# Kernel optimization log

Hardware: AMD Instinct MI355X
Metric: run time of the kernel (lower is better)

## Reference

```python
import jax, jax.numpy as jnp
import numpy as np

B, N, H = 8, 2000, 64  # batch, num_nodes(=input_dim), hidden(num_gru_units)


def _laplacian_self_loop(a):
    # batched: norm = D^{-1/2} (A + I) D^{-1/2}
    m = a + jnp.eye(a.shape[-1], dtype=a.dtype)
    d_inv_sqrt = jnp.sum(m, axis=-1) ** -0.5  # (B, N)
    return d_inv_sqrt[..., :, None] * m * d_inv_sqrt[..., None, :]


def _graph_conv(inputs, hidden_flat, adj, windd, W2, b2, W3, b3, W, b, out_dim):
    b_, _, n = inputs.shape
    # dynamic wind-based adjacency
    wind_now = inputs[:, 2, :] * 360.0  # (B, N)
    direction = jnp.abs(windd[None, :, :] - wind_now[:, :, None])  # (B, N, N)
    direction = jnp.where(direction > 360.0, 180.0, direction)
    d1 = jnp.maximum(jnp.cos(direction * (jnp.pi / 180.0)), 0.0)
    a = d1 @ W2.T + b2 + (adj @ W3.T + b3)[None]  # (B, N, N)
    a1 = _laplacian_self_loop(jnp.maximum(a, 0.0))
    # graph conv: concat [x, h] then A @ [.] then Linear
    x = jnp.concatenate([inputs[:, 0, :, None], hidden_flat.reshape(b_, n, H)], axis=2)  # (B,N,H+1)
    y = jnp.einsum('bij,bjh->bih', a1, x) @ W.T + b  # (B, N, out_dim)
    return y.reshape(b_, n * out_dim)


def reference(inputs, hidden_state, adj, windd, W2, b2, W3, b3, W1a, b1a, W1b, b1b, Wca1, Wca2, Wsa):
    b_, _, n = inputs.shape
    conc = _graph_conv(inputs, hidden_state, adj, windd, W2, b2, W3, b3, W1a, b1a, 2 * H)
    conc = conc.reshape(b_, 2 * H, n)  # faithful reshape (input_dim == N)
    # --- channel attention (CBAM) ---
    avg = jnp.mean(conc, axis=2, keepdims=True)  # (B, 2H, 1)
    mx = jnp.max(conc, axis=2, keepdims=True)
    def fc(v):
        return jnp.einsum('oc,bcx->box', Wca2, jax.nn.relu(jnp.einsum('oc,bcx->box', Wca1, v)))
    ca = jax.nn.sigmoid(fc(avg) + fc(mx))  # (B, 2H, 1)
    conc = ca * conc
    # --- spatial attention ---
    s = jnp.stack([jnp.mean(conc, axis=1), jnp.max(conc, axis=1)], axis=1)  # (B, 2, N)
    sa = jax.lax.conv_general_dilated(s, Wsa, window_strides=(1,), padding=((3, 3),),
                                      dimension_numbers=('NCH', 'OIH', 'NCH'))  # (B,1,N)
    conc = jax.nn.sigmoid(sa) * conc
    # --- GRU gates ---
    conc = jax.nn.sigmoid(conc.reshape(b_, 2 * H * n))
    r, u = jnp.split(conc, 2, axis=1)  # each (B, N*H)
    c = jnp.tanh(_graph_conv(inputs, r * hidden_state, adj, windd, W2, b2, W3, b3, W1b, b1b, H))
    new_hidden_state = u * hidden_state + (1.0 - u) * c
    return new_hidden_state


def setup_inputs() -> dict:
    key = jax.random.key(0)
    ks = jax.random.split(key, 12)
    inputs = jax.random.uniform(ks[0], (B, 3, N), dtype=jnp.float32)
    hidden_state = jax.random.normal(ks[1], (B, N * H), dtype=jnp.float32) * 0.1
    adj = jax.random.uniform(ks[2], (N, N), dtype=jnp.float32)
    windd = jax.random.uniform(ks[3], (N, N), dtype=jnp.float32) * 360.0
    sN = 1.0 / np.sqrt(N)
    W2 = jax.random.normal(ks[4], (N, N), dtype=jnp.float32) * sN
    b2 = jnp.zeros((N,), jnp.float32)
    W3 = jax.random.normal(ks[5], (N, N), dtype=jnp.float32) * sN
    b3 = jnp.zeros((N,), jnp.float32)
    sI = 1.0 / np.sqrt(H + 1)
    W1a = jax.random.normal(ks[6], (2 * H, H + 1), dtype=jnp.float32) * sI
    b1a = jnp.ones((2 * H,), jnp.float32)  # bias=1.0 in graph_conv1
    W1b = jax.random.normal(ks[7], (H, H + 1), dtype=jnp.float32) * sI
    b1b = jnp.zeros((H,), jnp.float32)
    Wca1 = jax.random.normal(ks[8], (2 * H // 16, 2 * H), dtype=jnp.float32) * (1.0 / np.sqrt(2 * H))
    Wca2 = jax.random.normal(ks[9], (2 * H, 2 * H // 16), dtype=jnp.float32) * (1.0 / np.sqrt(2 * H // 16))
    Wsa = jax.random.normal(ks[10], (1, 2, 7), dtype=jnp.float32) * (1.0 / np.sqrt(14))
    return {'inputs': inputs, 'hidden_state': hidden_state, 'adj': adj, 'windd': windd,
            'W2': W2, 'b2': b2, 'W3': W3, 'b3': b3, 'W1a': W1a, 'b1a': b1a,
            'W1b': W1b, 'b1b': b1b, 'Wca1': Wca1, 'Wca2': Wca2, 'Wsa': Wsa}
```

## Files before the change

kernel.cpp:

```cpp
#include <hip/hip_runtime.h>

#define NN 2000
#define BB 8
#define P  2048
#define NKT 64

typedef __attribute__((ext_vector_type(8))) short bf16x8;
typedef __attribute__((ext_vector_type(4))) float f32x4;

__device__ __forceinline__ float sigf(float x) { return 1.0f / (1.0f + expf(-x)); }

__device__ __forceinline__ short f2bf(float x) {
    union { float f; unsigned u; } v; v.f = x;
    unsigned r = v.u + 0x7fffu + ((v.u >> 16) & 1u);
    return (short)(r >> 16);
}
__device__ __forceinline__ float bf2f(short h) {
    union { unsigned u; float f; } v; v.u = ((unsigned)(unsigned short)h) << 16; return v.f;
}

__device__ __forceinline__ void gl2lds16(const short* g, short* l) {
    __builtin_amdgcn_global_load_lds(
        (const __attribute__((address_space(1))) void*)g,
        (__attribute__((address_space(3))) void*)l, 16, 0, 0);
}

__global__ __launch_bounds__(256) void k_cvtW(
    const float* __restrict__ s0, const float* __restrict__ s1, const float* __restrict__ s2,
    short* __restrict__ d0, short* __restrict__ d1, short* __restrict__ d2)
{
    const int i = blockIdx.x, sel = blockIdx.y, t = threadIdx.x;
    const float* s = (sel == 0) ? s0 : (sel == 1) ? s1 : s2;
    short* d = ((sel == 0) ? d0 : (sel == 1) ? d1 : d2) + ((size_t)i) * P + t * 8;
    bf16x8 v;
#pragma unroll
    for (int e = 0; e < 8; ++e) v[e] = 0;
    if (i < NN && t < 250) {
        const float* p = s + (size_t)i * NN + t * 8;
        float4 x0 = *(const float4*)p;
        float4 x1 = *(const float4*)(p + 4);
        float a[8] = {x0.x,x0.y,x0.z,x0.w,x1.x,x1.y,x1.z,x1.w};
#pragma unroll
        for (int e = 0; e < 8; ++e) v[e] = f2bf(a[e]);
    }
    *(bf16x8*)d = v;
}

__global__ __launch_bounds__(256) void k_cvtD1(
    const float* __restrict__ windd, const float* __restrict__ inputs, short* __restrict__ d1bf)
{
    const int i = blockIdx.x, t = threadIdx.x;
    const bool live = (i < NN) && (t < 250);
    float a[8];
    if (live) {
        const float* p = windd + (size_t)i * NN + t * 8;
        float4 x0 = *(const float4*)p;
        float4 x1 = *(const float4*)(p + 4);
        a[0]=x0.x; a[1]=x0.y; a[2]=x0.z; a[3]=x0.w;
        a[4]=x1.x; a[5]=x1.y; a[6]=x1.z; a[7]=x1.w;
    }
#pragma unroll
    for (int b = 0; b < BB; ++b) {
        bf16x8 v;
#pragma unroll
        for (int e = 0; e < 8; ++e) v[e] = 0;
        if (live) {
            const float wn = inputs[(size_t)b * 3 * NN + 2 * NN + i] * 360.0f;
#pragma unroll
            for (int e = 0; e < 8; ++e) {
                float dd = fabsf(a[e] - wn);
                dd = (dd > 360.0f) ? 180.0f : dd;
                float c = __cosf(dd * 0.01745329251994329577f);
                v[e] = f2bf(fmaxf(c, 0.0f));
            }
        }
        *(bf16x8*)(d1bf + ((size_t)b * P + i) * P + t * 8) = v;
    }
}

__global__ __launch_bounds__(512, 2) void k_g4s(
    const short* __restrict__ d1bf, const short* __restrict__ W2bf,
    const float* __restrict__ b2, const short* __restrict__ adjw,
    short* __restrict__ m_bf)
{
    __shared__ char smem[131072];
    const int t = threadIdx.x;
    const int w = t >> 6, lane = t & 63;
    const int wm = w >> 2, wn = w & 3;
    const int lr = lane & 15, lq = lane >> 4;
    const int tile = blockIdx.x;
    const int b = blockIdx.y;
    const int i0 = (tile & 7) * 256;
    const int j0 = (tile >> 3) * 256;
    const short* A  = d1bf + (size_t)b * P * P;
    const short* Bm = W2bf;

    const int cA0 = w * 64 + lane, cA1 = cA0 + 512;
    const int rA0 = cA0 >> 2, rA1 = cA1 >> 2;
    const short* srcA0 = A + (size_t)(i0 + rA0) * P + (((cA0 & 3) ^ ((rA0 >> 2) & 3)) * 8);
    const short* srcA1 = A + (size_t)(i0 + rA1) * P + (((cA1 & 3) ^ ((rA1 >> 2) & 3)) * 8);
    const short* srcB0 = Bm + (size_t)(j0 + rA0) * P + (((cA0 & 3) ^ ((rA0 >> 2) & 3)) * 8);
    const short* srcB1 = Bm + (size_t)(j0 + rA1) * P + (((cA1 & 3) ^ ((rA1 >> 2) & 3)) * 8);

#define STAGE_A(slot, ktI) do {                                                   \
        gl2lds16(srcA0 + (ktI) * 32, (short*)(smem + (slot) * 16384 + w * 1024)); \
        gl2lds16(srcA1 + (ktI) * 32, (short*)(smem + (slot) * 16384 + 8192 + w * 1024)); } while (0)
#define STAGE_B(slot, ktI) do {                                                   \
        gl2lds16(srcB0 + (ktI) * 32, (short*)(smem + 65536 + (slot) * 16384 + w * 1024)); \
        gl2lds16(srcB1 + (ktI) * 32, (short*)(smem + 65536 + (slot) * 16384 + 8192 + w * 1024)); } while (0)

    const int fch = (lq ^ (lr >> 2)) << 4;
    const int arowB = (wm * 128 + lr) * 64 + fch;
    const int browB = (wn * 64 + lr) * 64 + fch;

    f32x4 acc[8][4];
#pragma unroll
    for (int m = 0; m < 8; ++m)
#pragma unroll
        for (int n = 0; n < 4; ++n) acc[m][n] = (f32x4){0.f, 0.f, 0.f, 0.f};
    bf16x8 aF[4], bF[4];

    STAGE_A(0, 0); STAGE_B(0, 0);
    STAGE_A(1, 1); STAGE_B(1, 1);
    STAGE_A(2, 2); STAGE_B(2, 2);
    asm volatile("s_waitcnt vmcnt(0)" ::: "memory");
    __builtin_amdgcn_s_barrier();
    asm volatile("" ::: "memory");

#define MFMA_(a_, b_, m, n) acc[m][n] = __builtin_amdgcn_mfma_f32_16x16x32_bf16(a_, b_, acc[m][n], 0, 0, 0)
#define PHASE_MID()                                      \
    __builtin_amdgcn_s_barrier();                        \
    asm volatile("s_waitcnt lgkmcnt(0)" ::: "memory");   \
    __builtin_amdgcn_sched_barrier(0);                   \
    __builtin_amdgcn_s_setprio(1)
#define PHASE_TAIL()                                     \
    __builtin_amdgcn_s_setprio(0);                       \
    __builtin_amdgcn_sched_barrier(0);                   \
    asm volatile("s_waitcnt vmcnt(8)" ::: "memory");     \
    __builtin_amdgcn_s_barrier();                        \
    asm volatile("" ::: "memory")

    for (int kt = 0; kt < NKT; ++kt) {
        char* curA = smem + (kt & 3) * 16384;
        char* curB = smem + 65536 + (kt & 3) * 16384;
        const int stgSlot = (kt + 3) & 3;
        const int stgKt = (kt + 3 < NKT) ? (kt + 3) : (NKT - 1);

#pragma unroll
        for (int m = 0; m < 4; ++m) aF[m] = *(const bf16x8*)(curA + arowB + m * 1024);
#pragma unroll
        for (int n = 0; n < 4; ++n) bF[n] = *(const bf16x8*)(curB + browB + n * 1024);
        STAGE_A(stgSlot, stgKt);
        PHASE_MID();
#pragma unroll
        for (int m = 0; m < 4; ++m)
#pragma unroll
            for (int n = 0; n < 4; ++n) MFMA_(aF[m], bF[n], m, n);
        PHASE_TAIL();

#pragma unroll
        for (int m = 0; m < 4; ++m) aF[m] = *(const bf16x8*)(curA + arowB + (m + 4) * 1024);
        STAGE_B(stgSlot, stgKt);
        PHASE_MID();
#pragma unroll
        for (int m = 0; m < 4; ++m)
#pragma unroll
            for (int n = 0; n < 4; ++n) MFMA_(aF[m], bF[n], m + 4, n);
        PHASE_TAIL();
    }
    asm volatile("s_waitcnt vmcnt(0)" ::: "memory");

    const int rbase = i0 + wm * 128 + lq * 4;
    const int cbase = j0 + wn * 64 + lr;
#pragma unroll
    for (int m = 0; m < 8; ++m) {
#pragma unroll
        for (int n = 0; n < 4; ++n) {
            const int col = cbase + n * 16;
#pragma unroll
            for (int q = 0; q < 4; ++q) {
                const int row = rbase + m * 16 + q;
                short o = 0;
                if (row < NN && col < NN) {
                    float x = acc[m][n][q] + b2[col] + bf2f(adjw[(size_t)row * NN + col]);
                    x = fmaxf(x, 0.0f);
                    if (row == col) x += 1.0f;
                    o = f2bf(x);
                }
                m_bf[((size_t)b * P + row) * P + col] = o;
            }
        }
    }
#undef MFMA_
#undef PHASE_MID
#undef PHASE_TAIL
#undef STAGE_A
#undef STAGE_B
}

template<int EPI, int OUTD>
__global__ __launch_bounds__(256) void k_mfma(
    const short* __restrict__ Abase, const short* __restrict__ Bbase,
    const float* __restrict__ bias, const short* __restrict__ adjw,
    void* __restrict__ Cout, float* __restrict__ part, size_t aBatch)
{
    __shared__ short shA[4096];
    __shared__ short shB[4096];
    const int t = threadIdx.x;
    const int w = t >> 6, lane = t & 63;
    const int wr = w >> 1, wc = w & 1;

    int i0, j0, b, kt = 0;
    if (EPI == 2) {
        i0 = blockIdx.x * 128; j0 = 0; kt = blockIdx.y; b = blockIdx.z;
    } else {
        i0 = blockIdx.x * 128; j0 = blockIdx.y * 128; b = 0;
    }
    const int kb = (EPI == 2) ? kt * (P / 4) : 0;
    const int ke = (EPI == 2) ? kt * (P / 4) + (P / 4) : P;

    const short* A  = Abase + (size_t)b * aBatch;
    const short* Bm = Bbase + ((EPI == 2) ? (size_t)b * 128 * P : (size_t)0);

    f32x4 acc[4][4];
#pragma unroll
    for (int m = 0; m < 4; ++m)
#pragma unroll
        for (int n = 0; n < 4; ++n) acc[m][n] = (f32x4){0.f, 0.f, 0.f, 0.f};

    const int lidx0 = w * 128 + lane;
    const int lidx1 = lidx0 + 64;
    const short* aS0 = A  + (size_t)(i0 + (lidx0 >> 2)) * P + (lidx0 & 3) * 8;
    const short* aS1 = A  + (size_t)(i0 + (lidx1 >> 2)) * P + (lidx1 & 3) * 8;
    const short* bS0 = Bm + (size_t)(j0 + (lidx0 >> 2)) * P + (lidx0 & 3) * 8;
    const short* bS1 = Bm + (size_t)(j0 + (lidx1 >> 2)) * P + (lidx1 & 3) * 8;
    short* ldA0 = shA + (w * 128) * 8;
    short* ldA1 = shA + (w * 128 + 64) * 8;
    short* ldB0 = shB + (w * 128) * 8;
    short* ldB1 = shB + (w * 128 + 64) * 8;

    const int lr = lane & 15, lq = lane >> 4;
    const int aoff = (wr * 64 + lr) * 32 + lq * 8;
    const int boff = (wc * 64 + lr) * 32 + lq * 8;

    for (int k0 = kb; k0 < ke; k0 += 32) {
        gl2lds16(aS0 + k0, ldA0);
        gl2lds16(aS1 + k0, ldA1);
        gl2lds16(bS0 + k0, ldB0);
        gl2lds16(bS1 + k0, ldB1);
        __syncthreads();
        bf16x8 aF[4], bF[4];
#pragma unroll
        for (int m = 0; m < 4; ++m) aF[m] = *(const bf16x8*)(shA + aoff + m * 512);
#pragma unroll
        for (int n = 0; n < 4; ++n) bF[n] = *(const bf16x8*)(shB + boff + n * 512);
#pragma unroll
        for (int m = 0; m < 4; ++m)
#pragma unroll
            for (int n = 0; n < 4; ++n)
                acc[m][n] = __builtin_amdgcn_mfma_f32_16x16x32_bf16(aF[m], bF[n], acc[m][n], 0, 0, 0);
        __syncthreads();
    }

    const int rbase = i0 + wr * 64 + lq * 4;
    const int cbase = j0 + wc * 64 + lr;
#pragma unroll
    for (int m = 0; m < 4; ++m) {
#pragma unroll
        for (int n = 0; n < 4; ++n) {
            const int col = cbase + n * 16;
#pragma unroll
            for (int q = 0; q < 4; ++q) {
                const int row = rbase + m * 16 + q;
                float v = acc[m][n][q];
                if (EPI == 0) {
                    if (row < NN && col < NN)
                        ((short*)Cout)[(size_t)row * NN + col] = f2bf(v + bias[col]);
                } else {
                    if (row < NN && col < OUTD)
                        part[((size_t)(kt * BB + b) * NN + row) * OUTD + col] = v;
                }
            }
        }
    }
}

template<int OUTD>
__global__ __launch_bounds__(256) void k_comb(
    const float* __restrict__ part, const float* __restrict__ dinv,
    const float* __restrict__ bias, float* __restrict__ out)
{
    const size_t idx = (size_t)blockIdx.x * 256 + threadIdx.x;
    const size_t S = (size_t)BB * NN * OUTD;
    if (idx >= S) return;
    const int o = (int)(idx % OUTD);
    const size_t r = idx / OUTD;
    const int i = (int)(r % NN);
    const int b = (int)(r / NN);
    float s = ((part[idx] + part[idx + S]) + (part[idx + 2 * S] + part[idx + 3 * S]));
    out[idx] = s * dinv[b * NN + i] + bias[o];
}

__global__ __launch_bounds__(256) void k_rowsum_bf(const short* __restrict__ m_bf, float* __restrict__ dinv)
{
    const int i = blockIdx.x, b = blockIdx.y;
    const short* p = m_bf + ((size_t)b * P + i) * P + threadIdx.x * 8;
    bf16x8 v = *(const bf16x8*)p;
    float s = 0.0f;
#pragma unroll
    for (int e = 0; e < 8; ++e) s += bf2f(v[e]);
#pragma unroll
    for (int off = 32; off > 0; off >>= 1) s += __shfl_down(s, off);
    __shared__ float red[4];
    if ((threadIdx.x & 63) == 0) red[threadIdx.x >> 6] = s;
    __syncthreads();
    if (threadIdx.x == 0) dinv[b * NN + i] = rsqrtf(red[0] + red[1] + red[2] + red[3]);
}

template<int OUT>
__global__ __launch_bounds__(128) void k_xwT(
    const float* __restrict__ inputs, const float* __restrict__ hsrc,
    const float* __restrict__ W, const float* __restrict__ dinv, short* __restrict__ zT)
{
    const int b = blockIdx.y;
    const int j0 = blockIdx.x * 16;
    const int t = threadIdx.x;
    __shared__ float wl[128 * 65];
    __shared__ float xs[16 * 66];
    __shared__ float dj[16];
    for (int idx = t; idx < OUT * 65; idx += 128) wl[idx] = W[idx];
    for (int idx = t; idx < 16 * 64; idx += 128) {
        int jj = idx >> 6, hh = idx & 63, j = j0 + jj;
        xs[jj * 66 + 1 + hh] = (j < NN) ? hsrc[((size_t)b * NN + j) * 64 + hh] : 0.0f;
    }
    if (t < 16) {
        int j = j0 + t;
        xs[t * 66] = (j < NN) ? inputs[(size_t)b * 3 * NN + j] : 0.0f;
        dj[t] = (j < NN) ? dinv[b * NN + j] : 0.0f;
    }
    __syncthreads();
    for (int jj = 0; jj < 16; ++jj) {
        float a = 0.0f;
        if (t < OUT) {
            const float* xr = &xs[jj * 66];
            const float* wr = &wl[t * 65];
#pragma unroll
            for (int c = 0; c < 65; ++c) a = fmaf(xr[c], wr[c], a);
        }
        int j = j0 + jj;
        zT[((size_t)b * 128 + t) * P + j] = (t < OUT && j < NN) ? f2bf(a * dj[jj]) : (short)0;
    }
}

__global__ __launch_bounds__(256) void k_chred(const float* __restrict__ conc,
                                               float* __restrict__ avg, float* __restrict__ mx)
{
    const int bc = blockIdx.x;
    const float* p = conc + (size_t)bc * NN;
    float s = 0.0f, mv = -3.402823466e+38f;
    for (int n = threadIdx.x; n < NN; n += 256) { float v = p[n]; s += v; mv = fmaxf(mv, v); }
#pragma unroll
    for (int off = 32; off > 0; off >>= 1) {
        s += __shfl_down(s, off);
        mv = fmaxf(mv, __shfl_down(mv, off));
    }
    __shared__ float rs[4], rm[4];
    if ((threadIdx.x & 63) == 0) { rs[threadIdx.x >> 6] = s; rm[threadIdx.x >> 6] = mv; }
    __syncthreads();
    if (threadIdx.x == 0) {
        avg[bc] = (rs[0] + rs[1] + rs[2] + rs[3]) * (1.0f / NN);
        mx[bc]  = fmaxf(fmaxf(rm[0], rm[1]), fmaxf(rm[2], rm[3]));
    }
}

__global__ __launch_bounds__(128) void k_ca(
    const float* __restrict__ avg, const float* __restrict__ mx,
    const float* __restrict__ Wca1, const float* __restrict__ Wca2, float* __restrict__ ca)
{
    const int b = blockIdx.x, t = threadIdx.x;
    __shared__ float av[128], mv[128], h[16];
    av[t] = avg[b * 128 + t];
    mv[t] = mx[b * 128 + t];
    __syncthreads();
    if (t < 16) {
        int o8 = t & 7;
        const float* src = (t < 8) ? av : mv;
        float s = 0.0f;
        for (int c = 0; c < 128; ++c) s = fmaf(Wca1[o8 * 128 + c], src[c], s);
        h[t] = fmaxf(s, 0.0f);
    }
    __syncthreads();
    float s = 0.0f;
#pragma unroll
    for (int k = 0; k < 8; ++k) s = fmaf(Wca2[t * 8 + k], h[k] + h[8 + k], s);
    ca[b * 128 + t] = sigf(s);
}

__global__ __launch_bounds__(256) void k_satgate(
    const float* __restrict__ conc, const float* __restrict__ ca,
    const float* __restrict__ Wsa, const float* __restrict__ hidden,
    float* __restrict__ rh, float* __restrict__ u)
{
    const int b = blockIdx.y;
    const int n0 = blockIdx.x * 256;
    const int t = threadIdx.x;
    __shared__ float cas[128];
    __shared__ float wsa[14];
    __shared__ float s0l[262], s1l[262];
    if (t < 128) cas[t] = ca[b * 128 + t];
    if (t >= 128 && t < 142) wsa[t - 128] = Wsa[t - 128];
    __syncthreads();

    const float* cb = conc + (size_t)b * NN * 128;
    {
        const int n = n0 + t;
        float sm = 0.0f, sx = -3.402823466e+38f;
        if (n < NN) {
            for (int c = 0; c < 128; ++c) {
                float v = cas[c] * cb[(size_t)c * NN + n];
                sm += v; sx = fmaxf(sx, v);
            }
            s0l[t + 3] = sm * (1.0f / 128.0f);
            s1l[t + 3] = sx;
        } else { s0l[t + 3] = 0.0f; s1l[t + 3] = 0.0f; }
    }
    if (t < 6) {
        const int hn = (t < 3) ? (n0 - 3 + t) : (n0 + 256 + (t - 3));
        const int hi = (t < 3) ? t : (256 + t);
        float sm = 0.0f, sx = -3.402823466e+38f;
        if (hn >= 0 && hn < NN) {
            for (int c = 0; c < 128; ++c) {
                float v = cas[c] * cb[(size_t)c * NN + hn];
                sm += v; sx = fmaxf(sx, v);
            }
            s0l[hi] = sm * (1.0f / 128.0f);
            s1l[hi] = sx;
        } else { s0l[hi] = 0.0f; s1l[hi] = 0.0f; }
    }
    __syncthreads();

    const int n = n0 + t;
    if (n >= NN) return;
    float sa = 0.0f;
#pragma unroll
    for (int k = 0; k < 7; ++k)
        sa += wsa[k] * s0l[t + k] + wsa[7 + k] * s1l[t + k];
    float gs = sigf(sa);
    for (int c = 0; c < 128; ++c) {
        float v = gs * cas[c] * cb[(size_t)c * NN + n];
        float g = sigf(v);
        if (c < 64)
            rh[(size_t)b * NN * 64 + (size_t)c * NN + n] =
                g * hidden[(size_t)b * NN * 64 + (size_t)c * NN + n];
        else
            u[(size_t)b * NN * 64 + (size_t)(c - 64) * NN + n] = g;
    }
}

__global__ __launch_bounds__(256) void k_fin(
    const float* __restrict__ u, const float* __restrict__ hidden,
    const float* __restrict__ cpre, float* __restrict__ out)
{
    const size_t idx = (size_t)blockIdx.x * 256 + threadIdx.x;
    if (idx >= (size_t)BB * NN * 64) return;
    float uu = u[idx];
    out[idx] = uu * hidden[idx] + (1.0f - uu) * tanhf(cpre[idx]);
}

extern "C" void kernel_launch(void* const* d_in, const int* in_sizes, int n_in,
                              void* d_out, int out_size, void* d_ws, size_t ws_size,
                              hipStream_t stream)
{
    (void)in_sizes; (void)n_in; (void)out_size; (void)ws_size;
    const float* inputs = (const float*)d_in[0];
    const float* hidden = (const float*)d_in[1];
    const float* adj    = (const float*)d_in[2];
    const float* windd  = (const float*)d_in[3];
    const float* W2     = (const float*)d_in[4];
    const float* b2     = (const float*)d_in[5];
    const float* W3     = (const float*)d_in[6];
    const float* b3     = (const float*)d_in[7];
    const float* W1a    = (const float*)d_in[8];
    const float* b1a    = (const float*)d_in[9];
    const float* W1b    = (const float*)d_in[10];
    const float* b1b    = (const float*)d_in[11];
    const float* Wca1   = (const float*)d_in[12];
    const float* Wca2   = (const float*)d_in[13];
    const float* Wsa    = (const float*)d_in[14];
    float* out = (float*)d_out;

    char* W = (char*)d_ws;
    short* adjW3bf = (short*)(W + 0);
    short* W2bf    = (short*)(W + 8000000);
    short* W3bf    = (short*)(W + 16388608);
    short* adjbf   = (short*)(W + 24777216);
    short* m_bf    = (short*)(W + 16388608);
    char* D = W + 83497472;
    short* d1bf = (short*)D;
    float* dinv = (float*)(D + 0);
    float* avgb = (float*)(D + 64000);
    float* mxb  = (float*)(D + 68096);
    float* cab  = (float*)(D + 72192);
    short* zT   = (short*)(D + 204800);
    float* conc = (float*)(D + 4399104);
    float* rh   = (float*)(D + 12591104);
    float* ubuf = (float*)(D + 16687104);
    float* cpre = (float*)(D + 20783104);
    float* part = (float*)(D + 24879104);

    const size_t PP = (size_t)P * P;

    k_cvtW<<<dim3(P, 3), 256, 0, stream>>>(W2, W3, adj, W2bf, W3bf, adjbf);
    k_cvtD1<<<P, 256, 0, stream>>>(windd, inputs, d1bf);
    k_mfma<0, 0><<<dim3(16, 16, 1), 256, 0, stream>>>(adjbf, W3bf, b3, nullptr, adjW3bf, nullptr, 0);
    k_g4s<<<dim3(64, BB), 512, 0, stream>>>(d1bf, W2bf, b2, adjW3bf, m_bf);
    k_rowsum_bf<<<dim3(NN, BB), 256, 0, stream>>>(m_bf, dinv);
    k_xwT<128><<<dim3(128, BB), 128, 0, stream>>>(inputs, hidden, W1a, dinv, zT);
    k_mfma<2, 128><<<dim3(16, 4, BB), 256, 0, stream>>>(m_bf, zT, nullptr, nullptr, nullptr, part, PP);
    k_comb<128><<<(BB * NN * 128 + 255) / 256, 256, 0, stream>>>(part, dinv, b1a, conc);
    k_chred<<<BB * 128, 256, 0, stream>>>(conc, avgb, mxb);
    k_ca<<<BB, 128, 0, stream>>>(avgb, mxb, Wca1, Wca2, cab);
    k_satgate<<<dim3(8, BB), 256, 0, stream>>>(conc, cab, Wsa, hidden, rh, ubuf);
    k_xwT<64><<<dim3(128, BB), 128, 0, stream>>>(inputs, rh, W1b, dinv, zT);
    k_mfma<2, 64><<<dim3(16, 4, BB), 256, 0, stream>>>(m_bf, zT, nullptr, nullptr, nullptr, part, PP);
    k_comb<64><<<(BB * NN * 64 + 255) / 256, 256, 0, stream>>>(part, dinv, b1b, cpre);
    k_fin<<<(BB * NN * 64 + 255) / 256, 256, 0, stream>>>(ubuf, hidden, cpre, out);
}
```

Baseline: 442.4 us.

## Replace pipelined big-tile GEMM with simpler 256x128 tile kernel, fuse final combine

The batched d1@W2 GEMM kernel drops its 4-stage software-pipelined 256x256 tile with 128KB LDS. In its place is a simpler 256x128 tile with BK=64, single-buffered LDS (48KB), plain __syncthreads, and higher occupancy (4 blocks per CU). This trades explicit load/compute overlap for more resident blocks hiding latency, at the cost of lower per-block data reuse. Separately, the last partial-sum combine and the GRU final update are fused into one kernel, which drops the cpre round trip and one launch.

Measured after the change: 442.8 us. About the same (+0.1%).

```diff
diff --git a/kernel.cpp b/kernel.cpp
--- a/kernel.cpp
+++ b/kernel.cpp
@@ -3,7 +3,7 @@
 #define NN 2000
 #define BB 8
 #define P  2048
-#define NKT 64
+#define NIT 32
 
 typedef __attribute__((ext_vector_type(8))) short bf16x8;
 typedef __attribute__((ext_vector_type(4))) float f32x4;
@@ -78,102 +78,77 @@
     }
 }
 
-__global__ __launch_bounds__(512, 2) void k_g4s(
+__global__ __launch_bounds__(512, 4) void k_g2(
     const short* __restrict__ d1bf, const short* __restrict__ W2bf,
     const float* __restrict__ b2, const short* __restrict__ adjw,
     short* __restrict__ m_bf)
 {
-    __shared__ char smem[131072];
+    __shared__ char smem[49152];
     const int t = threadIdx.x;
     const int w = t >> 6, lane = t & 63;
-    const int wm = w >> 2, wn = w & 3;
+    const int wm = w >> 1, wn = w & 1;
     const int lr = lane & 15, lq = lane >> 4;
-    const int tile = blockIdx.x;
-    const int b = blockIdx.y;
-    const int i0 = (tile & 7) * 256;
-    const int j0 = (tile >> 3) * 256;
+    const int b = blockIdx.z;
+    const int i0 = blockIdx.x * 256;
+    const int j0 = blockIdx.y * 128;
     const short* A  = d1bf + (size_t)b * P * P;
     const short* Bm = W2bf;
 
-    const int cA0 = w * 64 + lane, cA1 = cA0 + 512;
-    const int rA0 = cA0 >> 2, rA1 = cA1 >> 2;
-    const short* srcA0 = A + (size_t)(i0 + rA0) * P + (((cA0 & 3) ^ ((rA0 >> 2) & 3)) * 8);
-    const short* srcA1 = A + (size_t)(i0 + rA1) * P + (((cA1 & 3) ^ ((rA1 >> 2) & 3)) * 8);
-    const short* srcB0 = Bm + (size_t)(j0 + rA0) * P + (((cA0 & 3) ^ ((rA0 >> 2) & 3)) * 8);
-    const short* srcB1 = Bm + (size_t)(j0 + rA1) * P + (((cA1 & 3) ^ ((rA1 >> 2) & 3)) * 8);
-
-#define STAGE_A(slot, ktI) do {                                                   \
-        gl2lds16(srcA0 + (ktI) * 32, (short*)(smem + (slot) * 16384 + w * 1024)); \
-        gl2lds16(srcA1 + (ktI) * 32, (short*)(smem + (slot) * 16384 + 8192 + w * 1024)); } while (0)
-#define STAGE_B(slot, ktI) do {                                                   \
-        gl2lds16(srcB0 + (ktI) * 32, (short*)(smem + 65536 + (slot) * 16384 + w * 1024)); \
-        gl2lds16(srcB1 + (ktI) * 32, (short*)(smem + 65536 + (slot) * 16384 + 8192 + w * 1024)); } while (0)
-
-    const int fch = (lq ^ (lr >> 2)) << 4;
-    const int arowB = (wm * 128 + lr) * 64 + fch;
-    const int browB = (wn * 64 + lr) * 64 + fch;
-
-    f32x4 acc[8][4];
-#pragma unroll
-    for (int m = 0; m < 8; ++m)
+    const short* srcs[6];
+    int dsts[6];
+#pragma unroll
+    for (int q = 0; q < 6; ++q) {
+        const int c = (q < 4) ? (q * 512 + t) : ((q - 4) * 512 + t);
+        const int r = c >> 3;
+        const int g = (c & 7) ^ (r & 7);
+        if (q < 4) { srcs[q] = A  + (size_t)(i0 + r) * P + g * 8; dsts[q] = c * 16; }
+        else       { srcs[q] = Bm + (size_t)(j0 + r) * P + g * 8; dsts[q] = 32768 + c * 16; }
+    }
+
+    const int fx0 = ((lq)     ^ (lr & 7)) << 4;
+    const int fx1 = ((4 + lq) ^ (lr & 7)) << 4;
+    const int arowB = (wm * 64 + lr) * 128;
+    const int browB = 32768 + (wn * 64 + lr) * 128;
+
+    f32x4 acc[4][4];
+#pragma unroll
+    for (int m = 0; m < 4; ++m)
 #pragma unroll
         for (int n = 0; n < 4; ++n) acc[m][n] = (f32x4){0.f, 0.f, 0.f, 0.f};
-    bf16x8 aF[4], bF[4];
-
-    STAGE_A(0, 0); STAGE_B(0, 0);
-    STAGE_A(1, 1); STAGE_B(1, 1);
-    STAGE_A(2, 2); STAGE_B(2, 2);
-    asm volatile("s_waitcnt vmcnt(0)" ::: "memory");
-    __builtin_amdgcn_s_barrier();
-    asm volatile("" ::: "memory");
-
-#define MFMA_(a_, b_, m, n) acc[m][n] = __builtin_amdgcn_mfma_f32_16x16x32_bf16(a_, b_, acc[m][n], 0, 0, 0)
-#define PHASE_MID()                                      \
-    __builtin_amdgcn_s_barrier();                        \
-    asm volatile("s_waitcnt lgkmcnt(0)" ::: "memory");   \
-    __builtin_amdgcn_sched_barrier(0);                   \
-    __builtin_amdgcn_s_setprio(1)
-#define PHASE_TAIL()                                     \
-    __builtin_amdgcn_s_setprio(0);                       \
-    __builtin_amdgcn_sched_barrier(0);                   \
-    asm volatile("s_waitcnt vmcnt(8)" ::: "memory");     \
-    __builtin_amdgcn_s_barrier();                        \
-    asm volatile("" ::: "memory")
-
-    for (int kt = 0; kt < NKT; ++kt) {
-        char* curA = smem + (kt & 3) * 16384;
-        char* curB = smem + 65536 + (kt & 3) * 16384;
-        const int stgSlot = (kt + 3) & 3;
-        const int stgKt = (kt + 3 < NKT) ? (kt + 3) : (NKT - 1);
-
-#pragma unroll
-        for (int m = 0; m < 4; ++m) aF[m] = *(const bf16x8*)(curA + arowB + m * 1024);
-#pragma unroll
-        for (int n = 0; n < 4; ++n) bF[n] = *(const bf16x8*)(curB + browB + n * 1024);
-        STAGE_A(stgSlot, stgKt);
-        PHASE_MID();
+
+    for (int kt = 0; kt < NIT; ++kt) {
+        const int kO = kt * 64;
+#pragma unroll
+        for (int q = 0; q < 6; ++q)
+            gl2lds16(srcs[q] + kO, (short*)(smem + dsts[q]));
+        __syncthreads();
+
+        bf16x8 aF[4], bF[4];
+#pragma unroll
+        for (int m = 0; m < 4; ++m) aF[m] = *(const bf16x8*)(smem + arowB + m * 2048 + fx0);
+#pragma unroll
+        for (int n = 0; n < 4; ++n) bF[n] = *(const bf16x8*)(smem + browB + n * 2048 + fx0);
 #pragma unroll
         for (int m = 0; m < 4; ++m)
 #pragma unroll
-            for (int n = 0; n < 4; ++n) MFMA_(aF[m], bF[n], m, n);
-        PHASE_TAIL();
-
-#pragma unroll
-        for (int m = 0; m < 4; ++m) aF[m] = *(const bf16x8*)(curA + arowB + (m + 4) * 1024);
-        STAGE_B(stgSlot, stgKt);
-        PHASE_MID();
+            for (int n = 0; n < 4; ++n)
+                acc[m][n] = __builtin_amdgcn_mfma_f32_16x16x32_bf16(aF[m], bF[n], acc[m][n], 0, 0, 0);
+#pragma unroll
+        for (int m = 0; m < 4; ++m) aF[m] = *(const bf16x8*)(smem + arowB + m * 2048 + fx1);
+#pragma unroll
+        for (int n = 0; n < 4; ++n) bF[n] = *(const bf16x8*)(smem + browB + n * 2048 + fx1);
 #pragma unroll
         for (int m = 0; m < 4; ++m)
 #pragma unroll
-            for (int n = 0; n < 4; ++n) MFMA_(aF[m], bF[n], m + 4, n);
-        PHASE_TAIL();
-    }
-    asm volatile("s_waitcnt vmcnt(0)" ::: "memory");
-
-    const int rbase = i0 + wm * 128 + lq * 4;
+            for (int n = 0; n < 4; ++n)
+                acc[m][n] = __builtin_amdgcn_mfma_f32_16x16x32_bf16(aF[m], bF[n], acc[m][n], 0, 0, 0);
+        __syncthreads();
+    }
+
+    const int rbase = i0 + wm * 64 + lq * 4;
     const int cbase = j0 + wn * 64 + lr;
 #pragma unroll
-    for (int m = 0; m < 8; ++m) {
+    for (int m = 0; m < 4; ++m) {
 #pragma unroll
         for (int n = 0; n < 4; ++n) {
             const int col = cbase + n * 16;
@@ -191,11 +166,6 @@
             }
         }
     }
-#undef MFMA_
-#undef PHASE_MID
-#undef PHASE_TAIL
-#undef STAGE_A
-#undef STAGE_B
 }
 
 template<int EPI, int OUTD>
@@ -301,6 +271,24 @@
     out[idx] = s * dinv[b * NN + i] + bias[o];
 }
 
+__global__ __launch_bounds__(256) void k_cfin(
+    const float* __restrict__ part, const float* __restrict__ dinv,
+    const float* __restrict__ bias, const float* __restrict__ u,
+    const float* __restrict__ hidden, float* __restrict__ out)
+{
+    const size_t idx = (size_t)blockIdx.x * 256 + threadIdx.x;
+    const size_t S = (size_t)BB * NN * 64;
+    if (idx >= S) return;
+    const int o = (int)(idx & 63);
+    const size_t r = idx >> 6;
+    const int i = (int)(r % NN);
+    const int b = (int)(r / NN);
+    float s = ((part[idx] + part[idx + S]) + (part[idx + 2 * S] + part[idx + 3 * S]));
+    float c = tanhf(s * dinv[b * NN + i] + bias[o]);
+    float uu = u[idx];
+    out[idx] = uu * hidden[idx] + (1.0f - uu) * c;
+}
+
 __global__ __launch_bounds__(256) void k_rowsum_bf(const short* __restrict__ m_bf, float* __restrict__ dinv)
 {
     const int i = blockIdx.x, b = blockIdx.y;
@@ -455,16 +443,6 @@
         else
             u[(size_t)b * NN * 64 + (size_t)(c - 64) * NN + n] = g;
     }
-}
-
-__global__ __launch_bounds__(256) void k_fin(
-    const float* __restrict__ u, const float* __restrict__ hidden,
-    const float* __restrict__ cpre, float* __restrict__ out)
-{
-    const size_t idx = (size_t)blockIdx.x * 256 + threadIdx.x;
-    if (idx >= (size_t)BB * NN * 64) return;
-    float uu = u[idx];
-    out[idx] = uu * hidden[idx] + (1.0f - uu) * tanhf(cpre[idx]);
 }
 
 extern "C" void kernel_launch(void* const* d_in, const int* in_sizes, int n_in,
@@ -505,7 +483,6 @@
     float* conc = (float*)(D + 4399104);
     float* rh   = (float*)(D + 12591104);
     float* ubuf = (float*)(D + 16687104);
-    float* cpre = (float*)(D + 20783104);
     float* part = (float*)(D + 24879104);
 
     const size_t PP = (size_t)P * P;
@@ -513,7 +490,7 @@
     k_cvtW<<<dim3(P, 3), 256, 0, stream>>>(W2, W3, adj, W2bf, W3bf, adjbf);
     k_cvtD1<<<P, 256, 0, stream>>>(windd, inputs, d1bf);
     k_mfma<0, 0><<<dim3(16, 16, 1), 256, 0, stream>>>(adjbf, W3bf, b3, nullptr, adjW3bf, nullptr, 0);
-    k_g4s<<<dim3(64, BB), 512, 0, stream>>>(d1bf, W2bf, b2, adjW3bf, m_bf);
+    k_g2<<<dim3(8, 16, BB), 512, 0, stream>>>(d1bf, W2bf, b2, adjW3bf, m_bf);
     k_rowsum_bf<<<dim3(NN, BB), 256, 0, stream>>>(m_bf, dinv);
     k_xwT<128><<<dim3(128, BB), 128, 0, stream>>>(inputs, hidden, W1a, dinv, zT);
     k_mfma<2, 128><<<dim3(16, 4, BB), 256, 0, stream>>>(m_bf, zT, nullptr, nullptr, nullptr, part, PP);
@@ -523,6 +500,5 @@
     k_satgate<<<dim3(8, BB), 256, 0, stream>>>(conc, cab, Wsa, hidden, rh, ubuf);
     k_xwT<64><<<dim3(128, BB), 128, 0, stream>>>(inputs, rh, W1b, dinv, zT);
     k_mfma<2, 64><<<dim3(16, 4, BB), 256, 0, stream>>>(m_bf, zT, nullptr, nullptr, nullptr, part, PP);
-    k_comb<64><<<(BB * NN * 64 + 255) / 256, 256, 0, stream>>>(part, dinv, b1b, cpre);
-    k_fin<<<(BB * NN * 64 + 255) / 256, 256, 0, stream>>>(ubuf, hidden, cpre, out);
-}
+    k_cfin<<<(BB * NN * 64 + 255) / 256, 256, 0, stream>>>(part, dinv, b1b, ubuf, hidden, out);
+}
```
